# Kernel optimization log

Hardware: AMD Instinct MI355X
Metric: run time of the kernel (lower is better)

Reference implementation:

```python
import jax, jax.numpy as jnp
import numpy as np

EPS = 1e-06


def _phi(x):
    # elu_feature_map: elu(x) + 1  (strictly positive features)
    return jax.nn.elu(x) + 1.0


def setup_inputs() -> dict:
    key = jax.random.key(0)
    k1, k2, k3 = jax.random.split(key, 3)
    N, L, H, D = 4, 4096, 12, 64
    q = jax.random.normal(k1, (N, L, H, D), dtype=jnp.float32)
    k = jax.random.normal(k2, (N, L, H, D), dtype=jnp.float32)
    v = jax.random.normal(k3, (N, L, H, D), dtype=jnp.float32)
    return {"q": q, "k": k, "v": v}


def _causal_linear_attention(q, k, v):
    qf = _phi(q)  # [N,L,H,D]
    kf = _phi(k)
    # normalizer: z_l = q_l . (sum_{s<=l} k_s) + eps
    z = jnp.einsum('nlhd,nlhd->nlh', qf, jnp.cumsum(kf, axis=1)) + EPS
    # causal_dot_product: sequential cumulative outer-product scan over L
    q_l = jnp.moveaxis(qf, 1, 0)  # [L,N,H,D]
    k_l = jnp.moveaxis(kf, 1, 0)
    v_l = jnp.moveaxis(v, 1, 0)   # [L,N,H,M]
    N, H, D = qf.shape[0], qf.shape[2], qf.shape[3]
    M = v.shape[3]
    S0 = jnp.zeros((N, H, D, M), dtype=qf.dtype)

    def step(S, qkv):
        ql, kl, vl = qkv
        S = S + jnp.einsum('nhd,nhm->nhdm', kl, vl)  # accumulate k v^T
        o = jnp.einsum('nhd,nhdm->nhm', ql, S)       # q . S
        return S, o

    _, out = jax.lax.scan(step, S0, (q_l, k_l, v_l))  # out: [L,N,H,M]
    out = jnp.moveaxis(out, 0, 1)  # [N,L,H,M]
    return out / z[..., None]


def reference(q, k, v):
    # mask=None path of LinearAttention.forward (causal linear attention)
    return _causal_linear_attention(q, k, v)
```

## Files before the change

### kernel.cpp

```cpp
#include <hip/hip_runtime.h>


#define NBATCH 4
#define LSEQ   4096
#define NHEAD  12
#define DDIM   64
#define LSTRIDE (NHEAD * DDIM)
#define NH     (NBATCH * NHEAD)
#define EPSF   1e-6f
#define CHUNK  64
#define NUMC   (LSEQ / CHUNK)
#define PPART  32
#define CPP    (NUMC / PPART)
#define SB     72

typedef __attribute__((ext_vector_type(8))) short bf16x8;
typedef __attribute__((ext_vector_type(4))) float f32x4;

__device__ __forceinline__ float phi(float x) { return x > 0.f ? x + 1.f : __expf(x); }
__device__ __forceinline__ float4 phi4(float4 x) {
    float4 r = {phi(x.x), phi(x.y), phi(x.z), phi(x.w)};
    return r;
}

__device__ __forceinline__ unsigned short f2bf(float x) {
    union { float f; unsigned u; } v; v.f = x;
    unsigned r = v.u + 0x7fffu + ((v.u >> 16) & 1u);
    return (unsigned short)(r >> 16);
}
__device__ __forceinline__ float bf2f(short s) {
    union { float f; unsigned u; } v; v.u = ((unsigned)(unsigned short)s) << 16;
    return v.f;
}
__device__ __forceinline__ uint2 pack4(float4 a) {
    uint2 r;
    r.x = (unsigned)f2bf(a.x) | ((unsigned)f2bf(a.y) << 16);
    r.y = (unsigned)f2bf(a.z) | ((unsigned)f2bf(a.w) << 16);
    return r;
}
__device__ __forceinline__ bf16x8 packbf8(float4 a, float4 b) {
    union { bf16x8 v; uint2 u[2]; } r;
    r.u[0] = pack4(a);
    r.u[1] = pack4(b);
    return r.v;
}

__device__ __forceinline__ float4 xpose4(float4 x, int lane) {
    const bool b0 = (lane >> 4) & 1, b1 = (lane >> 5) & 1;
    float s0 = b0 ? x.x : x.y;
    float s1 = b0 ? x.z : x.w;
    s0 = __shfl_xor(s0, 16);
    s1 = __shfl_xor(s1, 16);
    float4 y;
    if (b0) { y.x = s0;  y.y = x.y; y.z = s1;  y.w = x.w; }
    else    { y.x = x.x; y.y = s0;  y.z = x.z; y.w = s1;  }
    float t0 = b1 ? y.x : y.z;
    float t1 = b1 ? y.y : y.w;
    t0 = __shfl_xor(t0, 32);
    t1 = __shfl_xor(t1, 32);
    float4 z;
    if (b1) { z.x = t0;  z.y = t1;  z.z = y.z; z.w = y.w; }
    else    { z.x = y.x; z.y = y.y; z.z = t0;  z.w = t1;  }
    return z;
}

__global__ __launch_bounds__(256) void k_pass1(const float* __restrict__ qin,
                                               const float* __restrict__ kin,
                                               const float* __restrict__ vin,
                                               float* __restrict__ kvws,
                                               float* __restrict__ ksws,
                                               float* __restrict__ zws,
                                               float* __restrict__ out) {
    __shared__ short sK [64 * SB];
    __shared__ short sKT[64 * SB];
    __shared__ short sVT[64 * SB];
    __shared__ short sST[64 * SB];
    __shared__ float sKs[64];
    __shared__ float sZq[64];

    const int b = blockIdx.x, seq = b / PPART, p = b % PPART;
    const int n0 = seq / NHEAD, h0 = seq % NHEAD;
    const int t = threadIdx.x;
    const int lane = t & 63, w = t >> 6;
    const int nn = lane & 15, qq = lane >> 4;
    const int c4 = nn << 2;

    float4 kreg[4], vreg[4];
    auto LOADKV = [&](int cc) {
        const int gb = ((n0 * LSEQ + (p * CPP + cc) * CHUNK) * NHEAD + h0) * DDIM;
#pragma unroll
        for (int rep = 0; rep < 4; ++rep) {
            const int r16 = rep * 16 + 4 * w + qq;
            kreg[rep] = *(const float4*)(kin + gb + r16 * LSTRIDE + c4);
            vreg[rep] = *(const float4*)(vin + gb + r16 * LSTRIDE + c4);
        }
    };
    auto LOADQ = [&](int cc, bf16x8& o0, bf16x8& o1) {
        const float* qp = qin + ((n0 * LSEQ + (p * CPP + cc) * CHUNK) * NHEAD + h0) * DDIM
                        + (16 * w + nn) * LSTRIDE;
        float4 a = phi4(*(const float4*)(qp + qq * 8));
        float4 bq = phi4(*(const float4*)(qp + qq * 8 + 4));
        float4 cq = phi4(*(const float4*)(qp + 32 + qq * 8));
        float4 dq = phi4(*(const float4*)(qp + 32 + qq * 8 + 4));
        o0 = packbf8(a, bq);
        o1 = packbf8(cq, dq);
    };

    bf16x8 qf0, qf1, qfn0, qfn1;
    LOADKV(0);
    LOADQ(0, qf0, qf1);
    if (t < 64) sKs[t] = 0.f;

    f32x4 Sreg[4] = {{0,0,0,0},{0,0,0,0},{0,0,0,0},{0,0,0,0}};
    float ksTot = 0.f;

    for (int cc = 0; cc < CPP; ++cc) {
        const int gbase = ((n0 * LSEQ + (p * CPP + cc) * CHUNK) * NHEAD + h0) * DDIM;
#pragma unroll
        for (int rep = 0; rep < 4; ++rep) {
            const int row = rep * 16 + 4 * w + qq;
            const int l0 = rep * 16 + 4 * w;
            float4 kp = phi4(kreg[rep]);
            *(uint2*)(sK + row * SB + c4) = pack4(kp);
            float4 kt = xpose4(kp, lane);
            *(uint2*)(sKT + (c4 + qq) * SB + l0) = pack4(kt);
            float4 vt = xpose4(vreg[rep], lane);
            *(uint2*)(sVT + (c4 + qq) * SB + l0) = pack4(vt);
        }
        __syncthreads();

        if (cc + 1 < CPP) {
            LOADKV(cc + 1);
            LOADQ(cc + 1, qfn0, qfn1);
        }

        const int rowA = 16 * w + nn;
        float am[4][4];
        float zrow[4] = {0.f, 0.f, 0.f, 0.f};
#pragma unroll
        for (int ct = 0; ct < 4; ++ct) {
            bf16x8 kf0 = *(const bf16x8*)(sK + (16 * ct + nn) * SB + qq * 8);
            bf16x8 kf1 = *(const bf16x8*)(sK + (16 * ct + nn) * SB + 32 + qq * 8);
            f32x4 acc = {0.f, 0.f, 0.f, 0.f};
            acc = __builtin_amdgcn_mfma_f32_16x16x32_bf16(qf0, kf0, acc, 0, 0, 0);
            acc = __builtin_amdgcn_mfma_f32_16x16x32_bf16(qf1, kf1, acc, 0, 0, 0);
#pragma unroll
            for (int r = 0; r < 4; ++r) {
                const int ri = 16 * w + 4 * qq + r, cj = 16 * ct + nn;
                const float mval = (cj <= ri) ? acc[r] : 0.f;
                am[ct][r] = mval;
                zrow[r] += mval;
            }
        }
#pragma unroll
        for (int r = 0; r < 4; ++r) {
            float s = zrow[r];
            s += __shfl_xor(s, 1); s += __shfl_xor(s, 2);
            s += __shfl_xor(s, 4); s += __shfl_xor(s, 8);
            zrow[r] = s;
        }
        float zq = 0.f;
        if (cc) {
#pragma unroll
            for (int j = 0; j < 8; ++j) {
                zq += bf2f(qf0[j]) * sKs[qq * 8 + j];
                zq += bf2f(qf1[j]) * sKs[32 + qq * 8 + j];
            }
            zq += __shfl_xor(zq, 16);
            zq += __shfl_xor(zq, 32);
        }

        __syncthreads();
        if (qq == 0) sZq[16 * w + nn] = zq;
#pragma unroll
        for (int ct = 0; ct < 4; ++ct)
#pragma unroll
            for (int r = 0; r < 4; ++r)
                sK[(16 * w + 4 * qq + r) * SB + 16 * ct + nn] = (short)f2bf(am[ct][r]);
        __syncthreads();

        f32x4 o[4] = {{0,0,0,0},{0,0,0,0},{0,0,0,0},{0,0,0,0}};
        bf16x8 af0 = *(const bf16x8*)(sK + rowA * SB + qq * 8);
        bf16x8 af1 = *(const bf16x8*)(sK + rowA * SB + 32 + qq * 8);
        bf16x8 av0 = *(const bf16x8*)(sVT + rowA * SB + qq * 8);
        bf16x8 av1 = *(const bf16x8*)(sVT + rowA * SB + 32 + qq * 8);
        float ksc = 0.f;
#pragma unroll
        for (int ct = 0; ct < 4; ++ct) {
            bf16x8 vf0 = *(const bf16x8*)(sVT + (16 * ct + nn) * SB + qq * 8);
            bf16x8 vf1 = *(const bf16x8*)(sVT + (16 * ct + nn) * SB + 32 + qq * 8);
            o[ct] = __builtin_amdgcn_mfma_f32_16x16x32_bf16(af0, vf0, o[ct], 0, 0, 0);
            o[ct] = __builtin_amdgcn_mfma_f32_16x16x32_bf16(af1, vf1, o[ct], 0, 0, 0);
            if (cc) {
                bf16x8 sf0 = *(const bf16x8*)(sST + (16 * ct + nn) * SB + qq * 8);
                bf16x8 sf1 = *(const bf16x8*)(sST + (16 * ct + nn) * SB + 32 + qq * 8);
                o[ct] = __builtin_amdgcn_mfma_f32_16x16x32_bf16(qf0, sf0, o[ct], 0, 0, 0);
                o[ct] = __builtin_amdgcn_mfma_f32_16x16x32_bf16(qf1, sf1, o[ct], 0, 0, 0);
            }
            bf16x8 kt0 = *(const bf16x8*)(sKT + (16 * ct + nn) * SB + qq * 8);
            bf16x8 kt1 = *(const bf16x8*)(sKT + (16 * ct + nn) * SB + 32 + qq * 8);
            Sreg[ct] = __builtin_amdgcn_mfma_f32_16x16x32_bf16(av0, kt0, Sreg[ct], 0, 0, 0);
            Sreg[ct] = __builtin_amdgcn_mfma_f32_16x16x32_bf16(av1, kt1, Sreg[ct], 0, 0, 0);
            if (ct == w) {
                float s = 0.f;
#pragma unroll
                for (int j = 0; j < 8; ++j) s += bf2f(kt0[j]) + bf2f(kt1[j]);
                s += __shfl_xor(s, 16);
                s += __shfl_xor(s, 32);
                ksc = s;
            }
        }
        ksTot += ksc;

#pragma unroll
        for (int r = 0; r < 4; ++r) {
            const int ri = 16 * w + 4 * qq + r;
            if (nn == 0)
                zws[seq * LSEQ + (p * CPP + cc) * CHUNK + ri] = zrow[r] + sZq[ri];
#pragma unroll
            for (int ct = 0; ct < 4; ++ct)
                out[gbase + ri * LSTRIDE + 16 * ct + nn] = o[ct][r];
        }
        __syncthreads();
        if (cc + 1 < CPP) {
#pragma unroll
            for (int ct = 0; ct < 4; ++ct)
#pragma unroll
                for (int r = 0; r < 4; ++r)
                    sST[(16 * w + 4 * qq + r) * SB + 16 * ct + nn] = (short)f2bf(Sreg[ct][r]);
            if (qq == 0) sKs[16 * w + nn] += ksc;
            qf0 = qfn0;
            qf1 = qfn1;
        }
    }

    float* kvb = kvws + (size_t)b * (DDIM * DDIM);
#pragma unroll
    for (int ct = 0; ct < 4; ++ct)
#pragma unroll
        for (int r = 0; r < 4; ++r)
            kvb[(16 * w + 4 * qq + r) * DDIM + 16 * ct + nn] = Sreg[ct][r];
    if (qq == 0) ksws[b * DDIM + 16 * w + nn] = ksTot;
}

__global__ __launch_bounds__(64) void k_scanP(float* __restrict__ kv,
                                              float* __restrict__ ksum) {
    const int bid = blockIdx.x;
    const int seq = bid >> 4, part16 = bid & 15;
    const int t = threadIdx.x;
    float4* base = (float4*)(kv + (size_t)seq * PPART * DDIM * DDIM) + part16 * 64 + t;
    float4 S = {0.f, 0.f, 0.f, 0.f};
    for (int b0 = 0; b0 < PPART; b0 += 8) {
        float4 x[8];
#pragma unroll
        for (int j = 0; j < 8; ++j) x[j] = base[(b0 + j) * (DDIM * DDIM / 4)];
#pragma unroll
        for (int j = 0; j < 8; ++j) {
            base[(b0 + j) * (DDIM * DDIM / 4)] = S;
            S.x += x[j].x; S.y += x[j].y; S.z += x[j].z; S.w += x[j].w;
        }
    }
    if (part16 == 0) {
        float* kb = ksum + (size_t)seq * PPART * DDIM + t;
        float s = 0.f;
        for (int b0 = 0; b0 < PPART; b0 += 8) {
            float xs[8];
#pragma unroll
            for (int j = 0; j < 8; ++j) xs[j] = kb[(b0 + j) * DDIM];
#pragma unroll
            for (int j = 0; j < 8; ++j) { kb[(b0 + j) * DDIM] = s; s += xs[j]; }
        }
    }
}

__global__ __launch_bounds__(256) void k_fix(const float* __restrict__ qin,
                                             const float* __restrict__ kvws,
                                             const float* __restrict__ ksws,
                                             const float* __restrict__ zws,
                                             float* __restrict__ out) {
    __shared__ short sST[64 * SB];
    __shared__ float sKs[64];
    __shared__ float sZq[64];

    const int cg = blockIdx.x;
    const int seq = cg / NUMC, c = cg % NUMC, p = c / CPP;
    const int n0 = seq / NHEAD, h0 = seq % NHEAD;
    const int t = threadIdx.x;
    const int lane = t & 63, w = t >> 6;
    const int nn = lane & 15, qq = lane >> 4;
    const int c4 = nn << 2;
    const int gbase = ((n0 * LSEQ + c * CHUNK) * NHEAD + h0) * DDIM;

    if (t < 64) sKs[t] = ksws[(seq * PPART + p) * DDIM + t];

    const float* Sg = kvws + (size_t)(seq * PPART + p) * (DDIM * DDIM);
#pragma unroll
    for (int rep = 0; rep < 4; ++rep) {
        const int row = rep * 16 + 4 * w + qq;
        float4 sv = *(const float4*)(Sg + row * DDIM + c4);
        *(uint2*)(sST + row * SB + c4) = pack4(sv);
    }

    const float* qp = qin + gbase + (16 * w + nn) * LSTRIDE;
    float4 a  = phi4(*(const float4*)(qp + qq * 8));
    float4 bq = phi4(*(const float4*)(qp + qq * 8 + 4));
    float4 cq = phi4(*(const float4*)(qp + 32 + qq * 8));
    float4 dq = phi4(*(const float4*)(qp + 32 + qq * 8 + 4));
    bf16x8 qf0 = packbf8(a, bq);
    bf16x8 qf1 = packbf8(cq, dq);

    f32x4 o[4];
    float zl[4];
#pragma unroll
    for (int r = 0; r < 4; ++r) {
        const int ri = 16 * w + 4 * qq + r;
        zl[r] = zws[seq * LSEQ + c * CHUNK + ri];
#pragma unroll
        for (int ct = 0; ct < 4; ++ct)
            o[ct][r] = out[gbase + ri * LSTRIDE + 16 * ct + nn];
    }
    __syncthreads();

    float zq = 0.f;
#pragma unroll
    for (int j = 0; j < 8; ++j) {
        zq += bf2f(qf0[j]) * sKs[qq * 8 + j];
        zq += bf2f(qf1[j]) * sKs[32 + qq * 8 + j];
    }
    zq += __shfl_xor(zq, 16);
    zq += __shfl_xor(zq, 32);
    if (qq == 0) sZq[16 * w + nn] = zq;

#pragma unroll
    for (int ct = 0; ct < 4; ++ct) {
        bf16x8 sf0 = *(const bf16x8*)(sST + (16 * ct + nn) * SB + qq * 8);
        bf16x8 sf1 = *(const bf16x8*)(sST + (16 * ct + nn) * SB + 32 + qq * 8);
        o[ct] = __builtin_amdgcn_mfma_f32_16x16x32_bf16(qf0, sf0, o[ct], 0, 0, 0);
        o[ct] = __builtin_amdgcn_mfma_f32_16x16x32_bf16(qf1, sf1, o[ct], 0, 0, 0);
    }
    __syncthreads();

#pragma unroll
    for (int r = 0; r < 4; ++r) {
        const int ri = 16 * w + 4 * qq + r;
        const float z = zl[r] + sZq[ri] + EPSF;
        const float invz = 1.f / z;
#pragma unroll
        for (int ct = 0; ct < 4; ++ct)
            out[gbase + ri * LSTRIDE + 16 * ct + nn] = o[ct][r] * invz;
    }
}

__global__ __launch_bounds__(64) void k_seq(const float* __restrict__ qin,
                                            const float* __restrict__ kin,
                                            const float* __restrict__ vin,
                                            float* __restrict__ out) {
    const int seq = blockIdx.x;
    const int n = seq / NHEAD, h = seq % NHEAD;
    const int lane = threadIdx.x;
    float Scol[DDIM];
#pragma unroll
    for (int d = 0; d < DDIM; ++d) Scol[d] = 0.0f;
    float kc = 0.0f;
    __shared__ float qk[2 * DDIM];
    int base = (n * LSEQ * NHEAD + h) * DDIM + lane;
    for (int i = 0; i < LSEQ; ++i) {
        float qval = phi(qin[base]);
        float kval = phi(kin[base]);
        float vval = vin[base];
        kc += kval;
        float zp = qval * kc;
#pragma unroll
        for (int off = 32; off > 0; off >>= 1) zp += __shfl_xor(zp, off, 64);
        float z = zp + EPSF;
        qk[2 * lane] = kval;
        qk[2 * lane + 1] = qval;
        __syncthreads();
        const float4* qk4 = (const float4*)qk;
        float acc = 0.0f;
#pragma unroll
        for (int d2 = 0; d2 < DDIM / 2; ++d2) {
            float4 t0 = qk4[d2];
            int d = 2 * d2;
            Scol[d]     += t0.x * vval;  acc += t0.y * Scol[d];
            Scol[d + 1] += t0.z * vval;  acc += t0.w * Scol[d + 1];
        }
        out[base] = acc / z;
        base += LSTRIDE;
        __syncthreads();
    }
}

extern "C" void kernel_launch(void* const* d_in, const int* in_sizes, int n_in,
                              void* d_out, int out_size, void* d_ws, size_t ws_size,
                              hipStream_t stream) {
    const float* q = (const float*)d_in[0];
    const float* k = (const float*)d_in[1];
    const float* v = (const float*)d_in[2];
    float* out = (float*)d_out;
    float* ws  = (float*)d_ws;

    const size_t need = ((size_t)NH * PPART * (DDIM * DDIM + DDIM)
                        + (size_t)NH * LSEQ) * sizeof(float);
    if (ws_size >= need) {
        float* kv   = ws;
        float* ksum = kv + (size_t)NH * PPART * DDIM * DDIM;
        float* zws  = ksum + (size_t)NH * PPART * DDIM;
        k_pass1<<<NH * PPART, 256, 0, stream>>>(q, k, v, kv, ksum, zws, out);
        k_scanP<<<NH * 16,     64, 0, stream>>>(kv, ksum);
        k_fix  <<<NH * NUMC,  256, 0, stream>>>(q, kv, ksum, zws, out);
    } else {
        k_seq<<<NH, 64, 0, stream>>>(q, k, v, out);
    }
}
```

Baseline: 224.2 us.

## Swap MFMA operands to keep masked scores in registers and vectorize output stores

The MFMA operand order is swapped so each lane holds a full row's outputs. That lets the causally masked score tile be repacked into the A-operand layout with cross-lane shuffles instead of going through shared memory, which removes two block barriers and the sZq staging buffer per chunk. Output and fix-up loads and stores become 16-byte vector accesses per row rather than scalar strided ones, and the normalizer is reduced with a shorter shuffle chain. The cost is extra shuffle and select work and a more fragile layout correspondence that must match the MFMA fragment mapping.

```diff
diff --git a/kernel.cpp b/kernel.cpp
--- a/kernel.cpp
+++ b/kernel.cpp
@@ -64,6 +64,15 @@
     return z;
 }
 
+__device__ __forceinline__ void swapbit(uint2& A, uint2& B, int m, bool hi) {
+    uint2 t;
+    t.x = hi ? A.x : B.x;
+    t.y = hi ? A.y : B.y;
+    t.x = (unsigned)__shfl_xor((int)t.x, m);
+    t.y = (unsigned)__shfl_xor((int)t.y, m);
+    if (hi) { A.x = t.x; A.y = t.y; } else { B.x = t.x; B.y = t.y; }
+}
+
 __global__ __launch_bounds__(256) void k_pass1(const float* __restrict__ qin,
                                                const float* __restrict__ kin,
                                                const float* __restrict__ vin,
@@ -76,7 +85,6 @@
     __shared__ short sVT[64 * SB];
     __shared__ short sST[64 * SB];
     __shared__ float sKs[64];
-    __shared__ float sZq[64];
 
     const int b = blockIdx.x, seq = b / PPART, p = b % PPART;
     const int n0 = seq / NHEAD, h0 = seq % NHEAD;
@@ -84,6 +92,7 @@
     const int lane = t & 63, w = t >> 6;
     const int nn = lane & 15, qq = lane >> 4;
     const int c4 = nn << 2;
+    const bool b4 = (lane >> 4) & 1, b5 = (lane >> 5) & 1;
 
     float4 kreg[4], vreg[4];
     auto LOADKV = [&](int cc) {
@@ -113,6 +122,7 @@
 
     f32x4 Sreg[4] = {{0,0,0,0},{0,0,0,0},{0,0,0,0},{0,0,0,0}};
     float ksTot = 0.f;
+    const int iRow = 16 * w + nn;
 
     for (int cc = 0; cc < CPP; ++cc) {
         const int gbase = ((n0 * LSEQ + (p * CPP + cc) * CHUNK) * NHEAD + h0) * DDIM;
@@ -134,33 +144,28 @@
             LOADQ(cc + 1, qfn0, qfn1);
         }
 
-        const int rowA = 16 * w + nn;
-        float am[4][4];
-        float zrow[4] = {0.f, 0.f, 0.f, 0.f};
+        uint2 W[4];
+        float zpart = 0.f;
 #pragma unroll
         for (int ct = 0; ct < 4; ++ct) {
             bf16x8 kf0 = *(const bf16x8*)(sK + (16 * ct + nn) * SB + qq * 8);
             bf16x8 kf1 = *(const bf16x8*)(sK + (16 * ct + nn) * SB + 32 + qq * 8);
             f32x4 acc = {0.f, 0.f, 0.f, 0.f};
-            acc = __builtin_amdgcn_mfma_f32_16x16x32_bf16(qf0, kf0, acc, 0, 0, 0);
-            acc = __builtin_amdgcn_mfma_f32_16x16x32_bf16(qf1, kf1, acc, 0, 0, 0);
-#pragma unroll
-            for (int r = 0; r < 4; ++r) {
-                const int ri = 16 * w + 4 * qq + r, cj = 16 * ct + nn;
-                const float mval = (cj <= ri) ? acc[r] : 0.f;
-                am[ct][r] = mval;
-                zrow[r] += mval;
-            }
-        }
-#pragma unroll
-        for (int r = 0; r < 4; ++r) {
-            float s = zrow[r];
-            s += __shfl_xor(s, 1); s += __shfl_xor(s, 2);
-            s += __shfl_xor(s, 4); s += __shfl_xor(s, 8);
-            zrow[r] = s;
-        }
-        float zq = 0.f;
+            acc = __builtin_amdgcn_mfma_f32_16x16x32_bf16(kf0, qf0, acc, 0, 0, 0);
+            acc = __builtin_amdgcn_mfma_f32_16x16x32_bf16(kf1, qf1, acc, 0, 0, 0);
+            float4 mv;
+            mv.x = (16 * ct + 4 * qq + 0 <= iRow) ? acc[0] : 0.f;
+            mv.y = (16 * ct + 4 * qq + 1 <= iRow) ? acc[1] : 0.f;
+            mv.z = (16 * ct + 4 * qq + 2 <= iRow) ? acc[2] : 0.f;
+            mv.w = (16 * ct + 4 * qq + 3 <= iRow) ? acc[3] : 0.f;
+            zpart += mv.x + mv.y + mv.z + mv.w;
+            W[ct] = pack4(mv);
+        }
+        zpart += __shfl_xor(zpart, 16);
+        zpart += __shfl_xor(zpart, 32);
+        float zi = zpart;
         if (cc) {
+            float zq = 0.f;
 #pragma unroll
             for (int j = 0; j < 8; ++j) {
                 zq += bf2f(qf0[j]) * sKs[qq * 8 + j];
@@ -168,34 +173,35 @@
             }
             zq += __shfl_xor(zq, 16);
             zq += __shfl_xor(zq, 32);
-        }
-
-        __syncthreads();
-        if (qq == 0) sZq[16 * w + nn] = zq;
-#pragma unroll
-        for (int ct = 0; ct < 4; ++ct)
-#pragma unroll
-            for (int r = 0; r < 4; ++r)
-                sK[(16 * w + 4 * qq + r) * SB + 16 * ct + nn] = (short)f2bf(am[ct][r]);
-        __syncthreads();
+            zi += zq;
+        }
+
+        swapbit(W[0], W[1], 32, b5);
+        swapbit(W[2], W[3], 32, b5);
+        swapbit(W[0], W[1], 16, b4);
+        swapbit(W[2], W[3], 16, b4);
+        union U8 { unsigned u[4]; bf16x8 v; };
+        U8 a0, a1;
+        a0.u[0] = W[0].x; a0.u[1] = W[0].y; a0.u[2] = W[1].x; a0.u[3] = W[1].y;
+        a1.u[0] = W[2].x; a1.u[1] = W[2].y; a1.u[2] = W[3].x; a1.u[3] = W[3].y;
+        const bf16x8 amB0 = a0.v;
+        const bf16x8 amB1 = a1.v;
 
         f32x4 o[4] = {{0,0,0,0},{0,0,0,0},{0,0,0,0},{0,0,0,0}};
-        bf16x8 af0 = *(const bf16x8*)(sK + rowA * SB + qq * 8);
-        bf16x8 af1 = *(const bf16x8*)(sK + rowA * SB + 32 + qq * 8);
-        bf16x8 av0 = *(const bf16x8*)(sVT + rowA * SB + qq * 8);
-        bf16x8 av1 = *(const bf16x8*)(sVT + rowA * SB + 32 + qq * 8);
+        bf16x8 av0 = *(const bf16x8*)(sVT + iRow * SB + qq * 8);
+        bf16x8 av1 = *(const bf16x8*)(sVT + iRow * SB + 32 + qq * 8);
         float ksc = 0.f;
 #pragma unroll
         for (int ct = 0; ct < 4; ++ct) {
             bf16x8 vf0 = *(const bf16x8*)(sVT + (16 * ct + nn) * SB + qq * 8);
             bf16x8 vf1 = *(const bf16x8*)(sVT + (16 * ct + nn) * SB + 32 + qq * 8);
-            o[ct] = __builtin_amdgcn_mfma_f32_16x16x32_bf16(af0, vf0, o[ct], 0, 0, 0);
-            o[ct] = __builtin_amdgcn_mfma_f32_16x16x32_bf16(af1, vf1, o[ct], 0, 0, 0);
+            o[ct] = __builtin_amdgcn_mfma_f32_16x16x32_bf16(vf0, amB0, o[ct], 0, 0, 0);
+            o[ct] = __builtin_amdgcn_mfma_f32_16x16x32_bf16(vf1, amB1, o[ct], 0, 0, 0);
             if (cc) {
                 bf16x8 sf0 = *(const bf16x8*)(sST + (16 * ct + nn) * SB + qq * 8);
                 bf16x8 sf1 = *(const bf16x8*)(sST + (16 * ct + nn) * SB + 32 + qq * 8);
-                o[ct] = __builtin_amdgcn_mfma_f32_16x16x32_bf16(qf0, sf0, o[ct], 0, 0, 0);
-                o[ct] = __builtin_amdgcn_mfma_f32_16x16x32_bf16(qf1, sf1, o[ct], 0, 0, 0);
+                o[ct] = __builtin_amdgcn_mfma_f32_16x16x32_bf16(sf0, qf0, o[ct], 0, 0, 0);
+                o[ct] = __builtin_amdgcn_mfma_f32_16x16x32_bf16(sf1, qf1, o[ct], 0, 0, 0);
             }
             bf16x8 kt0 = *(const bf16x8*)(sKT + (16 * ct + nn) * SB + qq * 8);
             bf16x8 kt1 = *(const bf16x8*)(sKT + (16 * ct + nn) * SB + 32 + qq * 8);
@@ -212,15 +218,13 @@
         }
         ksTot += ksc;
 
-#pragma unroll
-        for (int r = 0; r < 4; ++r) {
-            const int ri = 16 * w + 4 * qq + r;
-            if (nn == 0)
-                zws[seq * LSEQ + (p * CPP + cc) * CHUNK + ri] = zrow[r] + sZq[ri];
-#pragma unroll
-            for (int ct = 0; ct < 4; ++ct)
-                out[gbase + ri * LSTRIDE + 16 * ct + nn] = o[ct][r];
-        }
+        float* orow = out + gbase + iRow * LSTRIDE;
+#pragma unroll
+        for (int ct = 0; ct < 4; ++ct)
+            *(f32x4*)(orow + 16 * ct + 4 * qq) = o[ct];
+        if (qq == 0)
+            zws[seq * LSEQ + (p * CPP + cc) * CHUNK + iRow] = zi;
+
         __syncthreads();
         if (cc + 1 < CPP) {
 #pragma unroll
@@ -280,7 +284,6 @@
                                              float* __restrict__ out) {
     __shared__ short sST[64 * SB];
     __shared__ float sKs[64];
-    __shared__ float sZq[64];
 
     const int cg = blockIdx.x;
     const int seq = cg / NUMC, c = cg % NUMC, p = c / CPP;
@@ -290,6 +293,7 @@
     const int nn = lane & 15, qq = lane >> 4;
     const int c4 = nn << 2;
     const int gbase = ((n0 * LSEQ + c * CHUNK) * NHEAD + h0) * DDIM;
+    const int iRow = 16 * w + nn;
 
     if (t < 64) sKs[t] = ksws[(seq * PPART + p) * DDIM + t];
 
@@ -301,7 +305,7 @@
         *(uint2*)(sST + row * SB + c4) = pack4(sv);
     }
 
-    const float* qp = qin + gbase + (16 * w + nn) * LSTRIDE;
+    const float* qp = qin + gbase + iRow * LSTRIDE;
     float4 a  = phi4(*(const float4*)(qp + qq * 8));
     float4 bq = phi4(*(const float4*)(qp + qq * 8 + 4));
     float4 cq = phi4(*(const float4*)(qp + 32 + qq * 8));
@@ -309,16 +313,12 @@
     bf16x8 qf0 = packbf8(a, bq);
     bf16x8 qf1 = packbf8(cq, dq);
 
+    float* orow = out + gbase + iRow * LSTRIDE;
     f32x4 o[4];
-    float zl[4];
-#pragma unroll
-    for (int r = 0; r < 4; ++r) {
-        const int ri = 16 * w + 4 * qq + r;
-        zl[r] = zws[seq * LSEQ + c * CHUNK + ri];
-#pragma unroll
-        for (int ct = 0; ct < 4; ++ct)
-            o[ct][r] = out[gbase + ri * LSTRIDE + 16 * ct + nn];
-    }
+#pragma unroll
+    for (int ct = 0; ct < 4; ++ct)
+        o[ct] = *(const f32x4*)(orow + 16 * ct + 4 * qq);
+    const float zl = zws[seq * LSEQ + c * CHUNK + iRow];
     __syncthreads();
 
     float zq = 0.f;
@@ -329,25 +329,21 @@
     }
     zq += __shfl_xor(zq, 16);
     zq += __shfl_xor(zq, 32);
-    if (qq == 0) sZq[16 * w + nn] = zq;
 
 #pragma unroll
     for (int ct = 0; ct < 4; ++ct) {
         bf16x8 sf0 = *(const bf16x8*)(sST + (16 * ct + nn) * SB + qq * 8);
         bf16x8 sf1 = *(const bf16x8*)(sST + (16 * ct + nn) * SB + 32 + qq * 8);
-        o[ct] = __builtin_amdgcn_mfma_f32_16x16x32_bf16(qf0, sf0, o[ct], 0, 0, 0);
-        o[ct] = __builtin_amdgcn_mfma_f32_16x16x32_bf16(qf1, sf1, o[ct], 0, 0, 0);
-    }
-    __syncthreads();
-
-#pragma unroll
-    for (int r = 0; r < 4; ++r) {
-        const int ri = 16 * w + 4 * qq + r;
-        const float z = zl[r] + sZq[ri] + EPSF;
-        const float invz = 1.f / z;
-#pragma unroll
-        for (int ct = 0; ct < 4; ++ct)
-            out[gbase + ri * LSTRIDE + 16 * ct + nn] = o[ct][r] * invz;
+        o[ct] = __builtin_amdgcn_mfma_f32_16x16x32_bf16(sf0, qf0, o[ct], 0, 0, 0);
+        o[ct] = __builtin_amdgcn_mfma_f32_16x16x32_bf16(sf1, qf1, o[ct], 0, 0, 0);
+    }
+
+    const float invz = 1.f / (zl + zq + EPSF);
+#pragma unroll
+    for (int ct = 0; ct < 4; ++ct) {
+        f32x4 r = o[ct];
+        r[0] *= invz; r[1] *= invz; r[2] *= invz; r[3] *= invz;
+        *(f32x4*)(orow + 16 * ct + 4 * qq) = r;
     }
 }
 
```

After: 224.5 us. About the same (+0.1%).
